# Performance work log

Hardware: AMD Instinct MI355X
Metric: run time of the kernel (lower is better)

## Reference

```python
import jax, jax.numpy as jnp
import numpy as np


def setup_inputs() -> dict:
    key = jax.random.key(0)
    bs, n_heads, ch, length = 4, 8, 64, 2048
    width = 3 * n_heads * ch  # 1536
    qkv = jax.random.normal(key, (bs, width, length), dtype=jnp.float32)
    return {"qkv": qkv, "n_heads": n_heads}


def reference(qkv, n_heads):
    bs, width, length = qkv.shape
    ch = width // (3 * n_heads)
    # reshape to (bs*heads, 3*ch, length) then split into q, k, v of (B, ch, L)
    qkv_r = qkv.reshape(bs * n_heads, 3 * ch, length)
    q, k, v = qkv_r[:, :ch], qkv_r[:, ch:2 * ch], qkv_r[:, 2 * ch:]
    scale = ch ** (-0.5)
    # weight = bmm(q^T, k) * scale -> (B, L_q, L_k)
    weight = jnp.einsum('bct,bcs->bts', q, k) * scale
    weight = jax.nn.softmax(weight.astype(jnp.float32), axis=-1).astype(qkv.dtype)
    # a = bmm(v, weight^T) -> (B, ch, L)
    a = jnp.einsum('bcs,bts->bct', v, weight)
    return a.reshape(bs, n_heads * ch, length)
```

## Files before the change

kernel.cpp:

```cpp
#include <hip/hip_runtime.h>

typedef __bf16 bf16;
typedef __attribute__((ext_vector_type(8)))  __bf16 bf16x8;
typedef __attribute__((ext_vector_type(16))) float  f32x16;

#define LEN   2048
#define CH    64
#define HEADS 32

union PackU { unsigned u[4]; bf16x8 v; };

static __device__ inline unsigned pack2(float lo, float hi) {
  union { bf16 h[2]; unsigned u; } p;
  p.h[0] = (bf16)lo; p.h[1] = (bf16)hi;
  return p.u;
}

static __device__ inline void async_cp16(const bf16* g, bf16* l) {
  __builtin_amdgcn_global_load_lds(
      (const __attribute__((address_space(1))) void*)g,
      (__attribute__((address_space(3))) void*)l, 16, 0, 0);
}

__global__ __launch_bounds__(256) void prep_kernel(const float* __restrict__ qkv,
                                                   bf16* __restrict__ ws) {
  __shared__ float tile[64][65];
  const int tIdx = blockIdx.x;
  const int g    = blockIdx.y;
  const int tid  = threadIdx.x;
  const int s0   = tIdx * 64;
  const float* K = qkv + (g * 192 + 64)  * LEN;
  const float* V = qkv + (g * 192 + 128) * LEN;

  {
    const int c0 = tid >> 6, s = tid & 63;
#pragma unroll
    for (int i = 0; i < 16; ++i) {
      const int c = c0 + i * 4;
      tile[c][s] = K[c * LEN + s0 + s];
    }
  }
  __syncthreads();

  bf16* dst = ws + ((size_t)g * 32 + tIdx) * 8192;
#pragma unroll
  for (int it = 0; it < 2; ++it) {
    const int c2  = tid + it * 256;
    const int row = c2 >> 3, cx = c2 & 7;
    const int k8  = cx ^ (row & 7) ^ ((row >> 3) & 7);
    const int cb  = k8 * 8;
    bf16x8 o;
#pragma unroll
    for (int j = 0; j < 8; ++j) o[j] = (bf16)tile[cb + j][row];
    *(bf16x8*)(dst + c2 * 8) = o;
  }
#pragma unroll
  for (int it = 0; it < 2; ++it) {
    const int c2  = tid + it * 256;
    const int row = c2 >> 3, cx = c2 & 7;
    const int k8  = cx ^ (row & 7) ^ ((row >> 3) & 7);
    const int pa  = 32 * (k8 >> 2) + 8 * ((k8 >> 1) & 1) + 4 * (k8 & 1);
    const float* src = V + row * LEN + s0 + pa;
    const float4 a = *(const float4*)src;
    const float4 b = *(const float4*)(src + 16);
    bf16x8 o;
    o[0] = (bf16)a.x; o[1] = (bf16)a.y; o[2] = (bf16)a.z; o[3] = (bf16)a.w;
    o[4] = (bf16)b.x; o[5] = (bf16)b.y; o[6] = (bf16)b.z; o[7] = (bf16)b.w;
    *(bf16x8*)(dst + 4096 + c2 * 8) = o;
  }
}

__global__ __launch_bounds__(512, 4) void attn_kernel(const float* __restrict__ qkv,
                                                      const bf16* __restrict__ ws,
                                                      float* __restrict__ out) {
  __shared__ __align__(16) bf16 stg[32768];

  const int tid  = threadIdx.x;
  const int lane = tid & 63;
  const int w    = tid >> 6;
  const int wg   = w & 1;
  const int eg   = (w >> 1) & 1;
  const int sg   = w >> 2;
  const int n    = lane & 31;
  const int h    = lane >> 5;
  const int g    = blockIdx.x & 31;
  const int jb   = blockIdx.x >> 5;
  const int t0   = jb * 128 + wg * 64;

  const bf16* wsg = ws + (size_t)g * (32 * 8192);

  auto stage = [&](int i) {
    const bf16* src = wsg + i * 8192;
    bf16* dst = stg + (i & 3) * 8192;
#pragma unroll
    for (int it = 0; it < 2; ++it) {
      const int chunk = w * 128 + it * 64 + lane;
      async_cp16(src + chunk * 8, dst + chunk * 8);
    }
  };
  stage(0); stage(1);

  const float qs = 0.125f * 1.44269504088896340736f;
  const float* Q = qkv + g * (192 * LEN);
  bf16x8 qf[4];
#pragma unroll
  for (int kb = 0; kb < 4; ++kb)
#pragma unroll
    for (int jj = 0; jj < 8; ++jj)
      qf[kb][jj] = (bf16)(Q[(kb * 16 + h * 8 + jj) * LEN + t0 + eg * 32 + n] * qs);

  f32x16 o_acc[2];
#pragma unroll
  for (int mb = 0; mb < 2; ++mb)
#pragma unroll
    for (int r = 0; r < 16; ++r) o_acc[mb][r] = 0.f;
  float l_acc = 0.f;

  for (int p = 0; p < 16; ++p) {
    __syncthreads();
    if (p < 15) { stage(2 * p + 2); stage(2 * p + 3); }
    const bf16* ktl = stg + ((2 * p + sg) & 3) * 8192;
    const bf16* vl  = ktl + 4096;

    f32x16 sf[2];
#pragma unroll
    for (int mb = 0; mb < 2; ++mb)
#pragma unroll
      for (int r = 0; r < 16; ++r) sf[mb][r] = 0.f;
#pragma unroll
    for (int kb = 0; kb < 4; ++kb)
#pragma unroll
      for (int mb = 0; mb < 2; ++mb) {
        const bf16x8 a = *(const bf16x8*)(ktl + (mb * 32 + n) * 64 +
                          (((kb * 2 + h) ^ (n & 7) ^ (mb << 2) ^ (n >> 3)) * 8));
        sf[mb] = __builtin_amdgcn_mfma_f32_32x32x16_bf16(a, qf[kb], sf[mb], 0, 0, 0);
      }

    PackU frag[4];
    float ls = 0.f;
#pragma unroll
    for (int mb = 0; mb < 2; ++mb)
#pragma unroll
      for (int u = 0; u < 4; ++u) {
        const float p0 = __builtin_amdgcn_exp2f(sf[mb][4 * u + 0]);
        const float p1 = __builtin_amdgcn_exp2f(sf[mb][4 * u + 1]);
        const float p2 = __builtin_amdgcn_exp2f(sf[mb][4 * u + 2]);
        const float p3 = __builtin_amdgcn_exp2f(sf[mb][4 * u + 3]);
        ls += (p0 + p1) + (p2 + p3);
        const int kb   = 2 * mb + (u & 1);
        const int base = 2 * (u >> 1);
        frag[kb].u[base]     = pack2(p0, p1);
        frag[kb].u[base + 1] = pack2(p2, p3);
      }
    l_acc += ls;

#pragma unroll
    for (int kbs = 0; kbs < 4; ++kbs)
#pragma unroll
      for (int mbo = 0; mbo < 2; ++mbo) {
        const bf16x8 a = *(const bf16x8*)(vl + (mbo * 32 + n) * 64 +
                          (((kbs * 2 + h) ^ (n & 7) ^ (mbo << 2) ^ (n >> 3)) * 8));
        o_acc[mbo] = __builtin_amdgcn_mfma_f32_32x32x16_bf16(a, frag[kbs].v, o_acc[mbo], 0, 0, 0);
      }
  }

  float lt = l_acc + __shfl_xor(l_acc, 32);

  float* fx = (float*)stg;
  float* lx = fx + 4608;

#pragma unroll
  for (int mbo = 0; mbo < 2; ++mbo) {
    __syncthreads();
    if (sg == 1) {
#pragma unroll
      for (int u = 0; u < 4; ++u) {
        float4 st;
        st.x = o_acc[mbo][4 * u + 0];
        st.y = o_acc[mbo][4 * u + 1];
        st.z = o_acc[mbo][4 * u + 2];
        st.w = o_acc[mbo][4 * u + 3];
        *(float4*)&fx[wg * 2304 + (eg * 32 + n) * 36 + 8 * u + 4 * h] = st;
      }
      if (mbo == 0 && h == 0) lx[wg * 64 + eg * 32 + n] = lt;
    }
    __syncthreads();
    if (sg == 0) {
#pragma unroll
      for (int u = 0; u < 4; ++u) {
        const float4 q = *(const float4*)&fx[wg * 2304 + (eg * 32 + n) * 36 + 8 * u + 4 * h];
        o_acc[mbo][4 * u + 0] += q.x;
        o_acc[mbo][4 * u + 1] += q.y;
        o_acc[mbo][4 * u + 2] += q.z;
        o_acc[mbo][4 * u + 3] += q.w;
      }
    }
  }

  if (sg == 0) {
    const float inv = 1.0f / (lt + lx[wg * 64 + eg * 32 + n]);
    float* og = out + g * (CH * LEN);
#pragma unroll
    for (int mbo = 0; mbo < 2; ++mbo)
#pragma unroll
      for (int r = 0; r < 16; ++r) {
        const int c = 32 * mbo + (r & 3) + 8 * (r >> 2) + 4 * h;
        og[c * LEN + t0 + eg * 32 + n] = o_acc[mbo][r] * inv;
      }
  }
}

extern "C" void kernel_launch(void* const* d_in, const int* in_sizes, int n_in,
                              void* d_out, int out_size, void* d_ws, size_t ws_size,
                              hipStream_t stream) {
  const float* qkv = (const float*)d_in[0];
  float* out = (float*)d_out;
  bf16* ws = (bf16*)d_ws;

  prep_kernel<<<dim3(32, HEADS), 256, 0, stream>>>(qkv, ws);
  attn_kernel<<<dim3(512), 512, 0, stream>>>(qkv, ws, out);
}
```

Before: 132.1 us.

## Software-pipeline PV MFMAs of previous tile with QK of current tile

Restructures the attention main loop so the P·V MFMAs for the previous key tile are issued alongside the Q·K MFMAs for the current tile. The V fragments are preloaded into registers, and the softmax exp/pack runs after the matrix work, so the dependency chain from QK to exp to PV no longer serialises inside one iteration. A prologue and epilogue handle the first and last tiles. s_setprio raises wave priority around the MFMA blocks. The extra V fragment registers raise register pressure under the 512-thread launch bound, which may cause spills or lower occupancy.

```diff
diff --git a/kernel.cpp b/kernel.cpp
--- a/kernel.cpp
+++ b/kernel.cpp
@@ -116,10 +116,13 @@
     for (int r = 0; r < 16; ++r) o_acc[mb][r] = 0.f;
   float l_acc = 0.f;
 
-  for (int p = 0; p < 16; ++p) {
-    __syncthreads();
-    if (p < 15) { stage(2 * p + 2); stage(2 * p + 3); }
-    const bf16* ktl = stg + ((2 * p + sg) & 3) * 8192;
+  PackU  frag[4];
+  bf16x8 vf[4][2];
+
+  {
+    __syncthreads();
+    stage(2); stage(3);
+    const bf16* ktl = stg + sg * 8192;
     const bf16* vl  = ktl + 4096;
 
     f32x16 sf[2];
@@ -135,8 +138,13 @@
                           (((kb * 2 + h) ^ (n & 7) ^ (mb << 2) ^ (n >> 3)) * 8));
         sf[mb] = __builtin_amdgcn_mfma_f32_32x32x16_bf16(a, qf[kb], sf[mb], 0, 0, 0);
       }
-
-    PackU frag[4];
+#pragma unroll
+    for (int kbs = 0; kbs < 4; ++kbs)
+#pragma unroll
+      for (int mbo = 0; mbo < 2; ++mbo)
+        vf[kbs][mbo] = *(const bf16x8*)(vl + (mbo * 32 + n) * 64 +
+                          (((kbs * 2 + h) ^ (n & 7) ^ (mbo << 2) ^ (n >> 3)) * 8));
+
     float ls = 0.f;
 #pragma unroll
     for (int mb = 0; mb < 2; ++mb)
@@ -153,16 +161,68 @@
         frag[kb].u[base + 1] = pack2(p2, p3);
       }
     l_acc += ls;
-
+  }
+
+  for (int p = 1; p < 16; ++p) {
+    __syncthreads();
+    if (p < 15) { stage(2 * p + 2); stage(2 * p + 3); }
+    const bf16* ktl = stg + ((2 * p + sg) & 3) * 8192;
+    const bf16* vl  = ktl + 4096;
+
+    __builtin_amdgcn_s_setprio(1);
 #pragma unroll
     for (int kbs = 0; kbs < 4; ++kbs)
 #pragma unroll
-      for (int mbo = 0; mbo < 2; ++mbo) {
-        const bf16x8 a = *(const bf16x8*)(vl + (mbo * 32 + n) * 64 +
+      for (int mbo = 0; mbo < 2; ++mbo)
+        o_acc[mbo] = __builtin_amdgcn_mfma_f32_32x32x16_bf16(vf[kbs][mbo], frag[kbs].v, o_acc[mbo], 0, 0, 0);
+
+    f32x16 sf[2];
+#pragma unroll
+    for (int mb = 0; mb < 2; ++mb)
+#pragma unroll
+      for (int r = 0; r < 16; ++r) sf[mb][r] = 0.f;
+#pragma unroll
+    for (int kb = 0; kb < 4; ++kb)
+#pragma unroll
+      for (int mb = 0; mb < 2; ++mb) {
+        const bf16x8 a = *(const bf16x8*)(ktl + (mb * 32 + n) * 64 +
+                          (((kb * 2 + h) ^ (n & 7) ^ (mb << 2) ^ (n >> 3)) * 8));
+        sf[mb] = __builtin_amdgcn_mfma_f32_32x32x16_bf16(a, qf[kb], sf[mb], 0, 0, 0);
+      }
+    __builtin_amdgcn_s_setprio(0);
+
+#pragma unroll
+    for (int kbs = 0; kbs < 4; ++kbs)
+#pragma unroll
+      for (int mbo = 0; mbo < 2; ++mbo)
+        vf[kbs][mbo] = *(const bf16x8*)(vl + (mbo * 32 + n) * 64 +
                           (((kbs * 2 + h) ^ (n & 7) ^ (mbo << 2) ^ (n >> 3)) * 8));
-        o_acc[mbo] = __builtin_amdgcn_mfma_f32_32x32x16_bf16(a, frag[kbs].v, o_acc[mbo], 0, 0, 0);
-      }
-  }
+
+    float ls = 0.f;
+#pragma unroll
+    for (int mb = 0; mb < 2; ++mb)
+#pragma unroll
+      for (int u = 0; u < 4; ++u) {
+        const float p0 = __builtin_amdgcn_exp2f(sf[mb][4 * u + 0]);
+        const float p1 = __builtin_amdgcn_exp2f(sf[mb][4 * u + 1]);
+        const float p2 = __builtin_amdgcn_exp2f(sf[mb][4 * u + 2]);
+        const float p3 = __builtin_amdgcn_exp2f(sf[mb][4 * u + 3]);
+        ls += (p0 + p1) + (p2 + p3);
+        const int kb   = 2 * mb + (u & 1);
+        const int base = 2 * (u >> 1);
+        frag[kb].u[base]     = pack2(p0, p1);
+        frag[kb].u[base + 1] = pack2(p2, p3);
+      }
+    l_acc += ls;
+  }
+
+  __builtin_amdgcn_s_setprio(1);
+#pragma unroll
+  for (int kbs = 0; kbs < 4; ++kbs)
+#pragma unroll
+    for (int mbo = 0; mbo < 2; ++mbo)
+      o_acc[mbo] = __builtin_amdgcn_mfma_f32_32x32x16_bf16(vf[kbs][mbo], frag[kbs].v, o_acc[mbo], 0, 0, 0);
+  __builtin_amdgcn_s_setprio(0);
 
   float lt = l_acc + __shfl_xor(l_acc, 32);
 
```

After: 136.1 us. 1.03x slower.

## Pre-swizzle K/V into MFMA fragment order and load directly from global

Applied to the files above, without the earlier changes.

The prep kernel now writes K and V tiles already laid out in per-lane MFMA operand order, so the attention kernel reads its fragments straight from global memory (L2) with coalesced 16-byte loads. This removes the LDS staging ring, the async copies, the per-iteration barriers and the split-K reduction through shared memory. Each wave now processes all 32 key tiles for 32 queries, with 256-thread blocks and s_setprio around the MFMA bursts. In exchange, every wave re-reads K/V from cache with no LDS reuse, and latency hiding now depends on occupancy rather than explicit prefetch.

```diff
diff --git a/kernel.cpp b/kernel.cpp
--- a/kernel.cpp
+++ b/kernel.cpp
@@ -14,12 +14,6 @@
   union { bf16 h[2]; unsigned u; } p;
   p.h[0] = (bf16)lo; p.h[1] = (bf16)hi;
   return p.u;
-}
-
-static __device__ inline void async_cp16(const bf16* g, bf16* l) {
-  __builtin_amdgcn_global_load_lds(
-      (const __attribute__((address_space(1))) void*)g,
-      (__attribute__((address_space(3))) void*)l, 16, 0, 0);
 }
 
 __global__ __launch_bounds__(256) void prep_kernel(const float* __restrict__ qkv,
@@ -45,22 +39,26 @@
   bf16* dst = ws + ((size_t)g * 32 + tIdx) * 8192;
 #pragma unroll
   for (int it = 0; it < 2; ++it) {
-    const int c2  = tid + it * 256;
-    const int row = c2 >> 3, cx = c2 & 7;
-    const int k8  = cx ^ (row & 7) ^ ((row >> 3) & 7);
-    const int cb  = k8 * 8;
+    const int c2 = tid + it * 256;
+    const int r  = c2 >> 6, ln = c2 & 63;
+    const int nn = ln & 31, hh = ln >> 5;
+    const int kb = r >> 1,  mb = r & 1;
+    const int s  = mb * 32 + nn;
+    const int cg = kb * 2 + hh;
     bf16x8 o;
 #pragma unroll
-    for (int j = 0; j < 8; ++j) o[j] = (bf16)tile[cb + j][row];
+    for (int j = 0; j < 8; ++j) o[j] = (bf16)tile[cg * 8 + j][s];
     *(bf16x8*)(dst + c2 * 8) = o;
   }
 #pragma unroll
   for (int it = 0; it < 2; ++it) {
     const int c2  = tid + it * 256;
-    const int row = c2 >> 3, cx = c2 & 7;
-    const int k8  = cx ^ (row & 7) ^ ((row >> 3) & 7);
+    const int r   = c2 >> 6, ln = c2 & 63;
+    const int nn  = ln & 31, hh = ln >> 5;
+    const int kbs = r >> 1,  mbo = r & 1;
+    const int k8  = kbs * 2 + hh;
     const int pa  = 32 * (k8 >> 2) + 8 * ((k8 >> 1) & 1) + 4 * (k8 & 1);
-    const float* src = V + row * LEN + s0 + pa;
+    const float* src = V + (mbo * 32 + nn) * LEN + s0 + pa;
     const float4 a = *(const float4*)src;
     const float4 b = *(const float4*)(src + 16);
     bf16x8 o;
@@ -70,35 +68,19 @@
   }
 }
 
-__global__ __launch_bounds__(512, 4) void attn_kernel(const float* __restrict__ qkv,
+__global__ __launch_bounds__(256, 2) void attn_kernel(const float* __restrict__ qkv,
                                                       const bf16* __restrict__ ws,
                                                       float* __restrict__ out) {
-  __shared__ __align__(16) bf16 stg[32768];
-
   const int tid  = threadIdx.x;
   const int lane = tid & 63;
-  const int w    = tid >> 6;
-  const int wg   = w & 1;
-  const int eg   = (w >> 1) & 1;
-  const int sg   = w >> 2;
+  const int wv   = tid >> 6;
   const int n    = lane & 31;
   const int h    = lane >> 5;
   const int g    = blockIdx.x & 31;
   const int jb   = blockIdx.x >> 5;
-  const int t0   = jb * 128 + wg * 64;
+  const int t0   = jb * 128 + wv * 32;
 
   const bf16* wsg = ws + (size_t)g * (32 * 8192);
-
-  auto stage = [&](int i) {
-    const bf16* src = wsg + i * 8192;
-    bf16* dst = stg + (i & 3) * 8192;
-#pragma unroll
-    for (int it = 0; it < 2; ++it) {
-      const int chunk = w * 128 + it * 64 + lane;
-      async_cp16(src + chunk * 8, dst + chunk * 8);
-    }
-  };
-  stage(0); stage(1);
 
   const float qs = 0.125f * 1.44269504088896340736f;
   const float* Q = qkv + g * (192 * LEN);
@@ -107,7 +89,7 @@
   for (int kb = 0; kb < 4; ++kb)
 #pragma unroll
     for (int jj = 0; jj < 8; ++jj)
-      qf[kb][jj] = (bf16)(Q[(kb * 16 + h * 8 + jj) * LEN + t0 + eg * 32 + n] * qs);
+      qf[kb][jj] = (bf16)(Q[(kb * 16 + h * 8 + jj) * LEN + t0 + n] * qs);
 
   f32x16 o_acc[2];
 #pragma unroll
@@ -116,25 +98,32 @@
     for (int r = 0; r < 16; ++r) o_acc[mb][r] = 0.f;
   float l_acc = 0.f;
 
-  for (int p = 0; p < 16; ++p) {
-    __syncthreads();
-    if (p < 15) { stage(2 * p + 2); stage(2 * p + 3); }
-    const bf16* ktl = stg + ((2 * p + sg) & 3) * 8192;
-    const bf16* vl  = ktl + 4096;
+  f32x16 zf;
+#pragma unroll
+  for (int r = 0; r < 16; ++r) zf[r] = 0.f;
+
+  for (int i = 0; i < 32; ++i) {
+    const bf16* tb = wsg + i * 8192;
+
+    bf16x8 ka[8], vf[8];
+#pragma unroll
+    for (int r = 0; r < 8; ++r)
+      ka[r] = *(const bf16x8*)(tb + r * 512 + lane * 8);
+#pragma unroll
+    for (int r = 0; r < 8; ++r)
+      vf[r] = *(const bf16x8*)(tb + 4096 + r * 512 + lane * 8);
 
     f32x16 sf[2];
+    __builtin_amdgcn_s_setprio(1);
 #pragma unroll
     for (int mb = 0; mb < 2; ++mb)
+      sf[mb] = __builtin_amdgcn_mfma_f32_32x32x16_bf16(ka[mb], qf[0], zf, 0, 0, 0);
 #pragma unroll
-      for (int r = 0; r < 16; ++r) sf[mb][r] = 0.f;
+    for (int kb = 1; kb < 4; ++kb)
 #pragma unroll
-    for (int kb = 0; kb < 4; ++kb)
-#pragma unroll
-      for (int mb = 0; mb < 2; ++mb) {
-        const bf16x8 a = *(const bf16x8*)(ktl + (mb * 32 + n) * 64 +
-                          (((kb * 2 + h) ^ (n & 7) ^ (mb << 2) ^ (n >> 3)) * 8));
-        sf[mb] = __builtin_amdgcn_mfma_f32_32x32x16_bf16(a, qf[kb], sf[mb], 0, 0, 0);
-      }
+      for (int mb = 0; mb < 2; ++mb)
+        sf[mb] = __builtin_amdgcn_mfma_f32_32x32x16_bf16(ka[kb * 2 + mb], qf[kb], sf[mb], 0, 0, 0);
+    __builtin_amdgcn_s_setprio(0);
 
     PackU frag[4];
     float ls = 0.f;
@@ -154,60 +143,25 @@
       }
     l_acc += ls;
 
+    __builtin_amdgcn_s_setprio(1);
 #pragma unroll
     for (int kbs = 0; kbs < 4; ++kbs)
 #pragma unroll
-      for (int mbo = 0; mbo < 2; ++mbo) {
-        const bf16x8 a = *(const bf16x8*)(vl + (mbo * 32 + n) * 64 +
-                          (((kbs * 2 + h) ^ (n & 7) ^ (mbo << 2) ^ (n >> 3)) * 8));
-        o_acc[mbo] = __builtin_amdgcn_mfma_f32_32x32x16_bf16(a, frag[kbs].v, o_acc[mbo], 0, 0, 0);
-      }
+      for (int mbo = 0; mbo < 2; ++mbo)
+        o_acc[mbo] = __builtin_amdgcn_mfma_f32_32x32x16_bf16(vf[kbs * 2 + mbo], frag[kbs].v, o_acc[mbo], 0, 0, 0);
+    __builtin_amdgcn_s_setprio(0);
   }
 
-  float lt = l_acc + __shfl_xor(l_acc, 32);
-
-  float* fx = (float*)stg;
-  float* lx = fx + 4608;
-
+  const float lt  = l_acc + __shfl_xor(l_acc, 32);
+  const float inv = 1.0f / lt;
+  float* og = out + g * (CH * LEN);
 #pragma unroll
-  for (int mbo = 0; mbo < 2; ++mbo) {
-    __syncthreads();
-    if (sg == 1) {
+  for (int mbo = 0; mbo < 2; ++mbo)
 #pragma unroll
-      for (int u = 0; u < 4; ++u) {
-        float4 st;
-        st.x = o_acc[mbo][4 * u + 0];
-        st.y = o_acc[mbo][4 * u + 1];
-        st.z = o_acc[mbo][4 * u + 2];
-        st.w = o_acc[mbo][4 * u + 3];
-        *(float4*)&fx[wg * 2304 + (eg * 32 + n) * 36 + 8 * u + 4 * h] = st;
-      }
-      if (mbo == 0 && h == 0) lx[wg * 64 + eg * 32 + n] = lt;
+    for (int r = 0; r < 16; ++r) {
+      const int c = 32 * mbo + (r & 3) + 8 * (r >> 2) + 4 * h;
+      og[c * LEN + t0 + n] = o_acc[mbo][r] * inv;
     }
-    __syncthreads();
-    if (sg == 0) {
-#pragma unroll
-      for (int u = 0; u < 4; ++u) {
-        const float4 q = *(const float4*)&fx[wg * 2304 + (eg * 32 + n) * 36 + 8 * u + 4 * h];
-        o_acc[mbo][4 * u + 0] += q.x;
-        o_acc[mbo][4 * u + 1] += q.y;
-        o_acc[mbo][4 * u + 2] += q.z;
-        o_acc[mbo][4 * u + 3] += q.w;
-      }
-    }
-  }
-
-  if (sg == 0) {
-    const float inv = 1.0f / (lt + lx[wg * 64 + eg * 32 + n]);
-    float* og = out + g * (CH * LEN);
-#pragma unroll
-    for (int mbo = 0; mbo < 2; ++mbo)
-#pragma unroll
-      for (int r = 0; r < 16; ++r) {
-        const int c = 32 * mbo + (r & 3) + 8 * (r >> 2) + 4 * h;
-        og[c * LEN + t0 + eg * 32 + n] = o_acc[mbo][r] * inv;
-      }
-  }
 }
 
 extern "C" void kernel_launch(void* const* d_in, const int* in_sizes, int n_in,
@@ -218,5 +172,5 @@
   bf16* ws = (bf16*)d_ws;
 
   prep_kernel<<<dim3(32, HEADS), 256, 0, stream>>>(qkv, ws);
-  attn_kernel<<<dim3(512), 512, 0, stream>>>(qkv, ws, out);
+  attn_kernel<<<dim3(512), 256, 0, stream>>>(qkv, ws, out);
 }
```

Result: no change. 131.2 us (-0.6%).
